# Optimization experiments

Hardware: AMD Instinct MI355X
Metric: run time of the kernel (lower is better)

Reference implementation:

```python
import jax, jax.numpy as jnp
import numpy as np

B, C_IN, H, T = 64, 256, 512, 1024
TMAX = 1024
EPS = 1e-5  # torch LayerNorm default


def setup_inputs() -> dict:
    key = jax.random.key(0)
    ks = jax.random.split(key, 8)
    std = 1.0 / np.sqrt(H)
    u = lambda k, shape: jax.random.uniform(k, shape, jnp.float32, -std, std)
    xs = jax.random.normal(ks[0], (B, C_IN, T), jnp.float32)
    # Linear weights (torch layout [out, in]); LayerNorm gamma=0.1, beta=0,
    # except h2h beta[H:2H] = log(Uniform(1, Tmax-1))  (chrono-style init).
    def ln_h2h_bias(k):
        b = jnp.zeros((3 * H,), jnp.float32)
        z = jnp.log(jax.random.uniform(k, (H,), jnp.float32, 1.0, TMAX - 1.0))
        return b.at[H:2 * H].set(z)
    gamma = jnp.full((3 * H,), 0.1, jnp.float32)
    beta0 = jnp.zeros((3 * H,), jnp.float32)
    return {
        "xs": xs,
        "Wx0": u(ks[1], (3 * H, C_IN)), "Wh0": u(ks[2], (3 * H, H)),
        "gx0": gamma, "bx0": beta0, "gh0": gamma, "bh0": ln_h2h_bias(ks[3]),
        "Wx1": u(ks[4], (3 * H, H)), "Wh1": u(ks[5], (3 * H, H)),
        "gx1": gamma, "bx1": beta0, "gh1": gamma, "bh1": ln_h2h_bias(ks[6]),
    }


def _ln(z, g, b):
    m = jnp.mean(z, axis=-1, keepdims=True)
    v = jnp.mean((z - m) ** 2, axis=-1, keepdims=True)
    return (z - m) * jax.lax.rsqrt(v + EPS) * g + b


def _cell(x, h, Wx, Wh, gx, bx, gh, bh):
    gate_x = _ln(x @ Wx.T, gx, bx)          # [B, 3H]
    gate_h = _ln(h @ Wh.T, gh, bh)          # [B, 3H]
    i_r, i_i, i_n = jnp.split(gate_x, 3, axis=-1)
    h_r, h_i, h_n = jnp.split(gate_h, 3, axis=-1)
    r = jax.nn.sigmoid(i_r + h_r)
    ig = jax.nn.sigmoid(i_i + h_i)
    n = jnp.tanh(i_n + r * h_n)
    return n + ig * (h - n)


def reference(xs, Wx0, Wh0, gx0, bx0, gh0, bh0, Wx1, Wh1, gx1, bx1, gh1, bh1):
    p0 = (Wx0, Wh0, gx0, bx0, gh0, bh0)
    p1 = (Wx1, Wh1, gx1, bx1, gh1, bh1)
    xs_t = jnp.transpose(xs, (2, 0, 1))  # [T, B, C_IN]
    h_init = (jnp.zeros((B, H), xs.dtype), jnp.zeros((B, H), xs.dtype))

    def step(carry, x):
        h0, h1 = carry
        h0 = _cell(x, h0, *p0)
        h1 = _cell(h0, h1, *p1)
        return (h0, h1), h1

    _, ys = jax.lax.scan(step, h_init, xs_t)  # [T, B, H]
    return jnp.transpose(ys, (1, 2, 0))       # [B, H, T]
```

## Files before the change

### kernel.cpp

```cpp
#include <hip/hip_runtime.h>
#include <hip/hip_bf16.h>
#include <cstdint>
#include <cstddef>


#define NBATCH 64
#define HDIM   512
#define THREE_H 1536
#define CINDIM 256
#define T_STEPS 1024
#define EPSLN 1e-5f
#define NBLK 64

typedef __bf16 bf8v __attribute__((ext_vector_type(8)));
typedef float f4 __attribute__((ext_vector_type(4)));
typedef float f2 __attribute__((ext_vector_type(2)));
typedef unsigned int u32x4 __attribute__((ext_vector_type(4)));

static constexpr size_t OFF_BAR    = 0;
static constexpr size_t OFF_ST0P   = 8192;
static constexpr size_t OFF_ST1P   = 24576;
static constexpr size_t OFF_ST2P   = 40960;
static constexpr size_t OFF_H0BF   = 57344;
static constexpr size_t OFF_H1BF   = 122880;
static constexpr size_t OFF_STATSX = 188416;
static constexpr size_t OFF_WH0HI  = 712704;
static constexpr size_t OFF_WH0LO  = OFF_WH0HI + 1572864;
static constexpr size_t OFF_WX1HI  = OFF_WH0LO + 1572864;
static constexpr size_t OFF_WX1LO  = OFF_WX1HI + 1572864;
static constexpr size_t OFF_WH1HI  = OFF_WX1LO + 1572864;
static constexpr size_t OFF_WH1LO  = OFF_WH1HI + 1572864;
static constexpr size_t OFF_WX0HI  = OFF_WH1LO + 1572864;
static constexpr size_t OFF_WX0LO  = OFF_WX0HI + 786432;
static constexpr size_t OFF_XST    = OFF_WX0LO + 786432;
static constexpr size_t OFF_GX0    = OFF_XST + 33554432;

__device__ __forceinline__ f4 mf(bf8v a, bf8v b, f4 c){
  return __builtin_amdgcn_mfma_f32_16x16x32_bf16(a, b, c, 0, 0, 0);
}
__device__ __forceinline__ float sigf(float x){ return 1.0f/(1.0f + __expf(-x)); }
__device__ __forceinline__ float tanhfast(float x){ return 1.0f - 2.0f/(__expf(2.0f*x) + 1.0f); }

__device__ __forceinline__ bf8v ld16_cross(const void* p){
  u32x4 t;
  asm volatile("global_load_dwordx4 %0, %1, off sc0 sc1" : "=v"(t) : "v"(p));
  return __builtin_bit_cast(bf8v, t);
}
__device__ __forceinline__ f4 ld16f_cross(const float* p){
  f4 v;
  asm volatile("global_load_dwordx4 %0, %1, off sc0 sc1" : "=v"(v) : "v"(p));
  return v;
}
__device__ __forceinline__ void st2_cross(__hip_bfloat16* p, unsigned int u){
  asm volatile("global_store_short %0, %1, off sc0 sc1" :: "v"(p), "v"(u));
}
__device__ __forceinline__ void st8f_cross(float* p, f2 v){
  asm volatile("global_store_dwordx2 %0, %1, off sc0 sc1" :: "v"(p), "v"(v));
}
__device__ __forceinline__ void vm_drain(){
  asm volatile("s_waitcnt vmcnt(0)" ::: "memory");
  __builtin_amdgcn_sched_barrier(0);
}

__device__ __forceinline__ void gbar(unsigned int* flags, unsigned int target){
  asm volatile("s_waitcnt vmcnt(0) lgkmcnt(0)" ::: "memory");
  __syncthreads();
  if (threadIdx.x == 0){
    unsigned int* myf = flags + (size_t)blockIdx.x * 32;
    asm volatile("global_store_dword %0, %1, off sc0 sc1" :: "v"(myf), "v"(target) : "memory");
  }
  const int lane = threadIdx.x & 63;
  const unsigned int* pf = flags + (size_t)lane * 32;
  for (;;){
    unsigned int v;
    asm volatile("global_load_dword %0, %1, off sc0 sc1\n\ts_waitcnt vmcnt(0)"
                 : "=v"(v) : "v"(pf) : "memory");
    if (__all((int)(v >= target))) break;
    __builtin_amdgcn_s_sleep(1);
  }
}

__global__ void k_zero(unsigned int* p, int nwords){
  for (int i = blockIdx.x*blockDim.x + threadIdx.x; i < nwords; i += gridDim.x*blockDim.x)
    p[i] = 0u;
}

__global__ void k_conv(const float* __restrict__ src, __hip_bfloat16* __restrict__ hi,
                       __hip_bfloat16* __restrict__ lo, int n){
  for (int i = blockIdx.x*blockDim.x + threadIdx.x; i < n; i += gridDim.x*blockDim.x){
    float w = src[i];
    __hip_bfloat16 h = __float2bfloat16(w);
    hi[i] = h;
    lo[i] = __float2bfloat16(w - __bfloat162float(h));
  }
}

__global__ void k_tr(const float* __restrict__ xs, __hip_bfloat16* __restrict__ xsT){
  const int total = NBATCH * CINDIM * (T_STEPS/4);
  for (int idx = blockIdx.x*blockDim.x + threadIdx.x; idx < total; idx += gridDim.x*blockDim.x){
    int b  = idx >> 16;
    int c  = (idx >> 8) & 255;
    int t4 = idx & 255;
    const float4 v = *(const float4*)(xs + ((size_t)b*CINDIM + c)*T_STEPS + t4*4);
    float vv[4] = {v.x, v.y, v.z, v.w};
    #pragma unroll
    for (int i = 0; i < 4; ++i)
      xsT[(size_t)(4*t4 + i)*(NBATCH*CINDIM) + b*CINDIM + c] = __float2bfloat16(vv[i]);
  }
}

__global__ __launch_bounds__(256,1) void k_xgemm(unsigned char* __restrict__ ws){
  const int tid = threadIdx.x;
  const int bx = blockIdx.x;
  const int t = bx >> 4, s = bx & 15;
  const int lane = tid & 63, w = tid >> 6, l15 = lane & 15, lg = lane >> 4;

  const __hip_bfloat16* X  = (const __hip_bfloat16*)(ws + OFF_XST) + (size_t)t*(NBATCH*CINDIM);
  const __hip_bfloat16* WH = (const __hip_bfloat16*)(ws + OFF_WX0HI);
  const __hip_bfloat16* WL = (const __hip_bfloat16*)(ws + OFF_WX0LO);
  float* statsX = (float*)(ws + OFF_STATSX);
  __hip_bfloat16* GX0 = (__hip_bfloat16*)(ws + OFF_GX0) + (size_t)t*(NBATCH*THREE_H);

  __shared__ __hip_bfloat16 SB[2][2][96][72];

  f4 acc[6];
  #pragma unroll
  for (int i = 0; i < 6; ++i) acc[i] = f4{0.f,0.f,0.f,0.f};

  bf8v A0[8];
  #pragma unroll
  for (int kk = 0; kk < 8; ++kk)
    A0[kk] = *(const bf8v*)(X + (16*w + l15)*CINDIM + kk*32 + 8*lg);

  bf8v pre[6];
  #pragma unroll
  for (int rep = 0; rep < 6; ++rep){
    int idx = tid + rep*256; int half = idx >= 768 ? 1 : 0; int i2 = idx - half*768;
    int rr = i2 >> 3, ko = (i2 & 7)*8;
    int j = 32*s + (rr & 31) + 512*(rr >> 5);
    const __hip_bfloat16* sp = (half ? WL : WH) + (size_t)j*CINDIM;
    pre[rep] = *(const bf8v*)(sp + ko);
  }
  #pragma unroll
  for (int chk = 0; chk < 4; ++chk){
    #pragma unroll
    for (int rep = 0; rep < 6; ++rep){
      int idx = tid + rep*256; int half = idx >= 768 ? 1 : 0; int i2 = idx - half*768;
      int rr = i2 >> 3, ko = (i2 & 7)*8;
      *(bf8v*)&SB[chk & 1][half][rr][ko] = pre[rep];
    }
    __syncthreads();
    if (chk < 3){
      #pragma unroll
      for (int rep = 0; rep < 6; ++rep){
        int idx = tid + rep*256; int half = idx >= 768 ? 1 : 0; int i2 = idx - half*768;
        int rr = i2 >> 3, ko = (i2 & 7)*8;
        int j = 32*s + (rr & 31) + 512*(rr >> 5);
        const __hip_bfloat16* sp = (half ? WL : WH) + (size_t)j*CINDIM;
        pre[rep] = *(const bf8v*)(sp + (chk+1)*64 + ko);
      }
    }
    #pragma unroll
    for (int sub = 0; sub < 2; ++sub){
      int kk = 2*chk + sub; int ko = 32*sub + 8*lg;
      bf8v a = A0[kk];
      #pragma unroll
      for (int nf = 0; nf < 6; ++nf){
        bf8v bh = *(const bf8v*)&SB[chk & 1][0][16*nf + l15][ko];
        bf8v bl = *(const bf8v*)&SB[chk & 1][1][16*nf + l15][ko];
        acc[nf] = mf(a, bh, acc[nf]);
        acc[nf] = mf(a, bl, acc[nf]);
      }
    }
  }

  #pragma unroll
  for (int r = 0; r < 4; ++r){
    int row = 16*w + 4*lg + r;
    float sm = 0.f, sq = 0.f;
    #pragma unroll
    for (int nf = 0; nf < 6; ++nf){
      float v = acc[nf][r];
      sm += v; sq += v*v;
      int tc = 16*nf + l15;
      int j = 32*s + (tc & 31) + 512*(tc >> 5);
      GX0[(size_t)row*THREE_H + j] = __float2bfloat16(v);
    }
    #pragma unroll
    for (int m = 1; m < 16; m <<= 1){ sm += __shfl_xor(sm, m); sq += __shfl_xor(sq, m); }
    if (l15 == 0){
      atomicAdd(&statsX[((size_t)t*64 + row)*2 + 0], sm);
      atomicAdd(&statsX[((size_t)t*64 + row)*2 + 1], sq);
    }
  }
}

__global__ void k_statsx(float* __restrict__ sx){
  int i = blockIdx.x*blockDim.x + threadIdx.x;
  if (i < T_STEPS*NBATCH){
    float s = sx[2*i], q = sx[2*i+1];
    float m = s * (1.0f/1536.0f);
    float v = fmaxf(q * (1.0f/1536.0f) - m*m, 0.0f);
    sx[2*i] = m;
    sx[2*i+1] = rsqrtf(v + EPSLN);
  }
}


__device__ __forceinline__ void runA(
    int s, unsigned char* ws, f4* red, f2* BC0,
    const float* gxg, const float* gxb, const float* ghg, const float* ghb)
{
  const int tid = threadIdx.x, lane = tid & 63, w = tid >> 6;
  const int l15 = lane & 15, lg = (lane >> 4) & 3;

  unsigned int* flags = (unsigned int*)(ws + OFF_BAR);
  float* st0P = (float*)(ws + OFF_ST0P);
  __hip_bfloat16* h0bf = (__hip_bfloat16*)(ws + OFF_H0BF);
  const float* statsX = (const float*)(ws + OFF_STATSX);
  const __hip_bfloat16* GX0 = (const __hip_bfloat16*)(ws + OFF_GX0);

  bf8v BW[3][4][2];
  {
    const __hip_bfloat16* hi = (const __hip_bfloat16*)(ws + OFF_WH0HI);
    const __hip_bfloat16* lo = (const __hip_bfloat16*)(ws + OFF_WH0LO);
    #pragma unroll
    for (int g = 0; g < 3; ++g){
      const size_t j = (size_t)(16*s + l15 + 512*g);
      #pragma unroll
      for (int kt = 0; kt < 4; ++kt){
        const size_t ko = (size_t)((4*w + kt)*32 + 8*lg);
        BW[g][kt][0] = *(const bf8v*)(hi + j*HDIM + ko);
        BW[g][kt][1] = *(const bf8v*)(lo + j*HDIM + ko);
      }
    }
  }
  float PXg[3], PXb[3], PHg[3], PHb[3];
  #pragma unroll
  for (int g = 0; g < 3; ++g){
    int j = 16*s + l15 + 512*g;
    PXg[g] = gxg[j]; PXb[g] = gxb[j]; PHg[g] = ghg[j]; PHb[g] = ghb[j];
  }

  float hp[4] = {0.f,0.f,0.f,0.f};
  unsigned int bc = 0;

  for (int tau = 0; tau <= T_STEPS; ++tau){
    const bool act = (tau < T_STEPS);
    f4 zx[3];
    float gxraw[3][4], mxv[4], rsxv[4];

    if (act){
      bf8v AR[4][4];
      #pragma unroll
      for (int rt = 0; rt < 4; ++rt)
        #pragma unroll
        for (int kt = 0; kt < 4; ++kt)
          AR[rt][kt] = ld16_cross(h0bf + (size_t)(16*rt + l15)*HDIM + (4*w + kt)*32 + 8*lg);
      vm_drain();

      f4 AC[3][4];
      #pragma unroll
      for (int g = 0; g < 3; ++g)
        #pragma unroll
        for (int rt = 0; rt < 4; ++rt) AC[g][rt] = f4{0.f,0.f,0.f,0.f};
      #pragma unroll
      for (int kt = 0; kt < 4; ++kt)
        #pragma unroll
        for (int g = 0; g < 3; ++g)
          #pragma unroll
          for (int rt = 0; rt < 4; ++rt){
            AC[g][rt] = mf(AR[rt][kt], BW[g][kt][0], AC[g][rt]);
            AC[g][rt] = mf(AR[rt][kt], BW[g][kt][1], AC[g][rt]);
          }

      #pragma unroll
      for (int r = 0; r < 4; ++r){
        int row = 16*w + 4*lg + r;
        mxv[r]  = statsX[((size_t)tau*64 + row)*2 + 0];
        rsxv[r] = statsX[((size_t)tau*64 + row)*2 + 1];
        #pragma unroll
        for (int g = 0; g < 3; ++g)
          gxraw[g][r] = __bfloat162float(
            GX0[(size_t)tau*(NBATCH*THREE_H) + (size_t)row*THREE_H + (16*s + l15 + 512*g)]);
      }

      #pragma unroll
      for (int g = 0; g < 3; ++g)
        #pragma unroll
        for (int rt = 0; rt < 4; ++rt)
          red[((w*3 + g)*4 + rt)*64 + lane] = AC[g][rt];
      __syncthreads();
      #pragma unroll
      for (int g = 0; g < 3; ++g){
        f4 a = red[((0*3 + g)*4 + w)*64 + lane];
        a += red[((1*3 + g)*4 + w)*64 + lane];
        a += red[((2*3 + g)*4 + w)*64 + lane];
        a += red[((3*3 + g)*4 + w)*64 + lane];
        zx[g] = a;
      }

      #pragma unroll
      for (int r = 0; r < 4; ++r){
        float s1 = zx[0][r] + zx[1][r] + zx[2][r];
        float q1 = zx[0][r]*zx[0][r] + zx[1][r]*zx[1][r] + zx[2][r]*zx[2][r];
        #pragma unroll
        for (int m = 1; m < 16; m <<= 1){ s1 += __shfl_xor(s1, m); q1 += __shfl_xor(q1, m); }
        if (l15 == 0){
          int row = 16*w + 4*lg + r;
          st8f_cross(st0P + ((size_t)row*32 + s)*2, f2{s1, q1});
        }
      }
    }

    gbar(flags, ++bc);

    if (act){
      {
        int row = tid >> 2, q = tid & 3;
        const float* bp = st0P + (size_t)row*64 + q*16;
        f4 v0 = ld16f_cross(bp),   v1 = ld16f_cross(bp+4);
        f4 v2 = ld16f_cross(bp+8), v3 = ld16f_cross(bp+12);
        vm_drain();
        float sm = v0[0]+v0[2]+v1[0]+v1[2]+v2[0]+v2[2]+v3[0]+v3[2];
        float sq = v0[1]+v0[3]+v1[1]+v1[3]+v2[1]+v2[3]+v3[1]+v3[3];
        sm += __shfl_xor(sm,1); sq += __shfl_xor(sq,1);
        sm += __shfl_xor(sm,2); sq += __shfl_xor(sq,2);
        if (q == 0){
          float m = sm*(1.0f/1536.0f);
          float vv = fmaxf(sq*(1.0f/1536.0f) - m*m, 0.0f);
          BC0[row] = f2{m, rsqrtf(vv + EPSLN)};
        }
      }
      __syncthreads();
      #pragma unroll
      for (int r = 0; r < 4; ++r){
        int row = 16*w + 4*lg + r;
        f2 mr = BC0[row];
        float m = mr[0], rs = mr[1];
        float ghr = (zx[0][r]-m)*rs*PHg[0] + PHb[0];
        float ghi = (zx[1][r]-m)*rs*PHg[1] + PHb[1];
        float ghn = (zx[2][r]-m)*rs*PHg[2] + PHb[2];
        float gxr = (gxraw[0][r] - mxv[r])*rsxv[r]*PXg[0] + PXb[0];
        float gxi = (gxraw[1][r] - mxv[r])*rsxv[r]*PXg[1] + PXb[1];
        float gxn = (gxraw[2][r] - mxv[r])*rsxv[r]*PXg[2] + PXb[2];
        float rg = sigf(gxr + ghr);
        float ig = sigf(gxi + ghi);
        float nn = tanhfast(gxn + rg*ghn);
        float hn = nn + ig*(hp[r] - nn);
        hp[r] = hn;
        __hip_bfloat16 hb = __float2bfloat16(hn);
        st2_cross(h0bf + (size_t)row*HDIM + 16*s + l15,
                  (unsigned int)*reinterpret_cast<unsigned short*>(&hb));
      }
    }

    gbar(flags, ++bc);
  }
}

__device__ __forceinline__ void runB(
    int s, unsigned char* ws, f4* red, f2* BC1, f2* BC2,
    const float* gxg, const float* gxb, const float* ghg, const float* ghb,
    float* out)
{
  const int tid = threadIdx.x, lane = tid & 63, w = tid >> 6;
  const int l15 = lane & 15, lg = (lane >> 4) & 3;

  unsigned int* flags = (unsigned int*)(ws + OFF_BAR);
  float* st1P = (float*)(ws + OFF_ST1P);
  float* st2P = (float*)(ws + OFF_ST2P);
  __hip_bfloat16* h0bf = (__hip_bfloat16*)(ws + OFF_H0BF);
  __hip_bfloat16* h1bf = (__hip_bfloat16*)(ws + OFF_H1BF);

  bf8v BW[6][4][2];
  {
    const __hip_bfloat16* hix = (const __hip_bfloat16*)(ws + OFF_WX1HI);
    const __hip_bfloat16* lox = (const __hip_bfloat16*)(ws + OFF_WX1LO);
    const __hip_bfloat16* hih = (const __hip_bfloat16*)(ws + OFF_WH1HI);
    const __hip_bfloat16* loh = (const __hip_bfloat16*)(ws + OFF_WH1LO);
    #pragma unroll
    for (int g = 0; g < 3; ++g){
      const size_t j = (size_t)(16*s + l15 + 512*g);
      #pragma unroll
      for (int kt = 0; kt < 4; ++kt){
        const size_t ko = (size_t)((4*w + kt)*32 + 8*lg);
        BW[g][kt][0]   = *(const bf8v*)(hix + j*HDIM + ko);
        BW[g][kt][1]   = *(const bf8v*)(lox + j*HDIM + ko);
        BW[3+g][kt][0] = *(const bf8v*)(hih + j*HDIM + ko);
        BW[3+g][kt][1] = *(const bf8v*)(loh + j*HDIM + ko);
      }
    }
  }
  float PXg[3], PXb[3], PHg[3], PHb[3];
  #pragma unroll
  for (int g = 0; g < 3; ++g){
    int j = 16*s + l15 + 512*g;
    PXg[g] = gxg[j]; PXb[g] = gxb[j]; PHg[g] = ghg[j]; PHb[g] = ghb[j];
  }

  float hp[4] = {0.f,0.f,0.f,0.f};
  unsigned int bc = 0;

  for (int tau = 0; tau <= T_STEPS; ++tau){
    const bool act = (tau >= 1);
    f4 zx[3], zh[3];

    if (act){
      bf8v AR[4][4];
      #pragma unroll
      for (int rt = 0; rt < 4; ++rt)
        #pragma unroll
        for (int kt = 0; kt < 4; ++kt)
          AR[rt][kt] = ld16_cross(h0bf + (size_t)(16*rt + l15)*HDIM + (4*w + kt)*32 + 8*lg);
      vm_drain();

      f4 AC[3][4];
      #pragma unroll
      for (int g = 0; g < 3; ++g)
        #pragma unroll
        for (int rt = 0; rt < 4; ++rt) AC[g][rt] = f4{0.f,0.f,0.f,0.f};
      #pragma unroll
      for (int kt = 0; kt < 4; ++kt)
        #pragma unroll
        for (int g = 0; g < 3; ++g)
          #pragma unroll
          for (int rt = 0; rt < 4; ++rt){
            AC[g][rt] = mf(AR[rt][kt], BW[g][kt][0], AC[g][rt]);
            AC[g][rt] = mf(AR[rt][kt], BW[g][kt][1], AC[g][rt]);
          }
      #pragma unroll
      for (int g = 0; g < 3; ++g)
        #pragma unroll
        for (int rt = 0; rt < 4; ++rt)
          red[((w*3 + g)*4 + rt)*64 + lane] = AC[g][rt];

      #pragma unroll
      for (int rt = 0; rt < 4; ++rt)
        #pragma unroll
        for (int kt = 0; kt < 4; ++kt)
          AR[rt][kt] = ld16_cross(h1bf + (size_t)(16*rt + l15)*HDIM + (4*w + kt)*32 + 8*lg);

      __syncthreads();
      #pragma unroll
      for (int g = 0; g < 3; ++g){
        f4 a = red[((0*3 + g)*4 + w)*64 + lane];
        a += red[((1*3 + g)*4 + w)*64 + lane];
        a += red[((2*3 + g)*4 + w)*64 + lane];
        a += red[((3*3 + g)*4 + w)*64 + lane];
        zx[g] = a;
      }
      __syncthreads();

      vm_drain();
      #pragma unroll
      for (int g = 0; g < 3; ++g)
        #pragma unroll
        for (int rt = 0; rt < 4; ++rt) AC[g][rt] = f4{0.f,0.f,0.f,0.f};
      #pragma unroll
      for (int kt = 0; kt < 4; ++kt)
        #pragma unroll
        for (int g = 0; g < 3; ++g)
          #pragma unroll
          for (int rt = 0; rt < 4; ++rt){
            AC[g][rt] = mf(AR[rt][kt], BW[3+g][kt][0], AC[g][rt]);
            AC[g][rt] = mf(AR[rt][kt], BW[3+g][kt][1], AC[g][rt]);
          }
      #pragma unroll
      for (int g = 0; g < 3; ++g)
        #pragma unroll
        for (int rt = 0; rt < 4; ++rt)
          red[((w*3 + g)*4 + rt)*64 + lane] = AC[g][rt];
      __syncthreads();
      #pragma unroll
      for (int g = 0; g < 3; ++g){
        f4 a = red[((0*3 + g)*4 + w)*64 + lane];
        a += red[((1*3 + g)*4 + w)*64 + lane];
        a += red[((2*3 + g)*4 + w)*64 + lane];
        a += red[((3*3 + g)*4 + w)*64 + lane];
        zh[g] = a;
      }

      #pragma unroll
      for (int r = 0; r < 4; ++r){
        float s1 = zx[0][r] + zx[1][r] + zx[2][r];
        float q1 = zx[0][r]*zx[0][r] + zx[1][r]*zx[1][r] + zx[2][r]*zx[2][r];
        float s2 = zh[0][r] + zh[1][r] + zh[2][r];
        float q2 = zh[0][r]*zh[0][r] + zh[1][r]*zh[1][r] + zh[2][r]*zh[2][r];
        #pragma unroll
        for (int m = 1; m < 16; m <<= 1){
          s1 += __shfl_xor(s1, m); q1 += __shfl_xor(q1, m);
          s2 += __shfl_xor(s2, m); q2 += __shfl_xor(q2, m);
        }
        if (l15 == 0){
          int row = 16*w + 4*lg + r;
          st8f_cross(st1P + ((size_t)row*32 + s)*2, f2{s1, q1});
          st8f_cross(st2P + ((size_t)row*32 + s)*2, f2{s2, q2});
        }
      }
    }

    gbar(flags, ++bc);

    if (act){
      const int t1 = tau - 1;
      {
        int row = tid >> 2, q = tid & 3;
        const float* b1 = st1P + (size_t)row*64 + q*16;
        const float* b2 = st2P + (size_t)row*64 + q*16;
        f4 a0 = ld16f_cross(b1),   a1 = ld16f_cross(b1+4);
        f4 a2 = ld16f_cross(b1+8), a3 = ld16f_cross(b1+12);
        f4 c0 = ld16f_cross(b2),   c1 = ld16f_cross(b2+4);
        f4 c2 = ld16f_cross(b2+8), c3 = ld16f_cross(b2+12);
        vm_drain();
        float s1 = a0[0]+a0[2]+a1[0]+a1[2]+a2[0]+a2[2]+a3[0]+a3[2];
        float q1 = a0[1]+a0[3]+a1[1]+a1[3]+a2[1]+a2[3]+a3[1]+a3[3];
        float s2 = c0[0]+c0[2]+c1[0]+c1[2]+c2[0]+c2[2]+c3[0]+c3[2];
        float q2 = c0[1]+c0[3]+c1[1]+c1[3]+c2[1]+c2[3]+c3[1]+c3[3];
        s1 += __shfl_xor(s1,1); q1 += __shfl_xor(q1,1);
        s1 += __shfl_xor(s1,2); q1 += __shfl_xor(q1,2);
        s2 += __shfl_xor(s2,1); q2 += __shfl_xor(q2,1);
        s2 += __shfl_xor(s2,2); q2 += __shfl_xor(q2,2);
        if (q == 0){
          float m1 = s1*(1.0f/1536.0f);
          float v1 = fmaxf(q1*(1.0f/1536.0f) - m1*m1, 0.0f);
          BC1[row] = f2{m1, rsqrtf(v1 + EPSLN)};
          float m2 = s2*(1.0f/1536.0f);
          float v2 = fmaxf(q2*(1.0f/1536.0f) - m2*m2, 0.0f);
          BC2[row] = f2{m2, rsqrtf(v2 + EPSLN)};
        }
      }
      __syncthreads();
      #pragma unroll
      for (int r = 0; r < 4; ++r){
        int row = 16*w + 4*lg + r;
        f2 m1 = BC1[row], m2 = BC2[row];
        float gxr = (zx[0][r] - m1[0])*m1[1]*PXg[0] + PXb[0];
        float gxi = (zx[1][r] - m1[0])*m1[1]*PXg[1] + PXb[1];
        float gxn = (zx[2][r] - m1[0])*m1[1]*PXg[2] + PXb[2];
        float ghr = (zh[0][r] - m2[0])*m2[1]*PHg[0] + PHb[0];
        float ghi = (zh[1][r] - m2[0])*m2[1]*PHg[1] + PHb[1];
        float ghn = (zh[2][r] - m2[0])*m2[1]*PHg[2] + PHb[2];
        float rg = sigf(gxr + ghr);
        float ig = sigf(gxi + ghi);
        float nn = tanhfast(gxn + rg*ghn);
        float hn = nn + ig*(hp[r] - nn);
        hp[r] = hn;
        int j = 16*s + l15;
        __hip_bfloat16 hb = __float2bfloat16(hn);
        st2_cross(h1bf + (size_t)row*HDIM + j,
                  (unsigned int)*reinterpret_cast<unsigned short*>(&hb));
        out[(size_t)row*(HDIM*T_STEPS) + (size_t)j*T_STEPS + t1] = hn;
      }
    }

    gbar(flags, ++bc);
  }
}

__global__ __launch_bounds__(256,1) void k_rnn(
    const float* __restrict__ gx0g, const float* __restrict__ gx0b,
    const float* __restrict__ gh0g, const float* __restrict__ gh0b,
    const float* __restrict__ gx1g, const float* __restrict__ gx1b,
    const float* __restrict__ gh1g, const float* __restrict__ gh1b,
    unsigned char* __restrict__ ws, float* __restrict__ out)
{
  __shared__ f4 red[4*3*4*64];
  __shared__ f2 BCa[64];
  __shared__ f2 BCb[64];

  const int bi = blockIdx.x;
  if (bi < 32)
    runA(bi, ws, red, BCa, gx0g, gx0b, gh0g, gh0b);
  else
    runB(bi - 32, ws, red, BCa, BCb, gx1g, gx1b, gh1g, gh1b, out);
}

extern "C" void kernel_launch(void* const* d_in, const int* in_sizes, int n_in,
                              void* d_out, int out_size, void* d_ws, size_t ws_size,
                              hipStream_t stream) {
  const float* xs  = (const float*)d_in[0];
  const float* Wx0 = (const float*)d_in[1];
  const float* Wh0 = (const float*)d_in[2];
  const float* gx0g = (const float*)d_in[3];
  const float* gx0b = (const float*)d_in[4];
  const float* gh0g = (const float*)d_in[5];
  const float* gh0b = (const float*)d_in[6];
  const float* Wx1 = (const float*)d_in[7];
  const float* Wh1 = (const float*)d_in[8];
  const float* gx1g = (const float*)d_in[9];
  const float* gx1b = (const float*)d_in[10];
  const float* gh1g = (const float*)d_in[11];
  const float* gh1b = (const float*)d_in[12];

  unsigned char* ws = (unsigned char*)d_ws;
  float* out = (float*)d_out;
  (void)in_sizes; (void)n_in; (void)out_size; (void)ws_size;

  k_zero<<<256, 256, 0, stream>>>((unsigned int*)ws, (int)(OFF_WH0HI/4));

  k_conv<<<512, 256, 0, stream>>>(Wh0, (__hip_bfloat16*)(ws+OFF_WH0HI), (__hip_bfloat16*)(ws+OFF_WH0LO), THREE_H*HDIM);
  k_conv<<<512, 256, 0, stream>>>(Wx1, (__hip_bfloat16*)(ws+OFF_WX1HI), (__hip_bfloat16*)(ws+OFF_WX1LO), THREE_H*HDIM);
  k_conv<<<512, 256, 0, stream>>>(Wh1, (__hip_bfloat16*)(ws+OFF_WH1HI), (__hip_bfloat16*)(ws+OFF_WH1LO), THREE_H*HDIM);
  k_conv<<<512, 256, 0, stream>>>(Wx0, (__hip_bfloat16*)(ws+OFF_WX0HI), (__hip_bfloat16*)(ws+OFF_WX0LO), THREE_H*CINDIM);

  k_tr<<<4096, 256, 0, stream>>>(xs, (__hip_bfloat16*)(ws+OFF_XST));

  k_xgemm<<<16384, 256, 0, stream>>>(ws);
  k_statsx<<<256, 256, 0, stream>>>((float*)(ws+OFF_STATSX));

  k_rnn<<<NBLK, 256, 0, stream>>>(gx0g, gx0b, gh0g, gh0b, gx1g, gx1b, gh1g, gh1b, ws, out);
}
```

Before: 13.02 ms.

## Replace per-step stats barriers with epoch-tagged partial polling and double-buffered hidden states

Partial LayerNorm sums are now written as 16-byte records tagged with the step index. Consumers spin on those tags instead of passing through a grid-wide flag barrier, which removes one of the two global barriers per time step. The hidden-state buffers for both layers are double-buffered by step parity so the remaining barrier still orders reads against writes. Layer B's final step is peeled out of the loop. The cost is more workspace, polling traffic on the stats arrays, and reliance on the float tag and the write landing atomically.

```diff
diff --git a/kernel.cpp b/kernel.cpp
--- a/kernel.cpp
+++ b/kernel.cpp
@@ -11,6 +11,7 @@
 #define T_STEPS 1024
 #define EPSLN 1e-5f
 #define NBLK 64
+#define HSZ (NBATCH*HDIM)
 
 typedef __bf16 bf8v __attribute__((ext_vector_type(8)));
 typedef float f4 __attribute__((ext_vector_type(4)));
@@ -18,13 +19,13 @@
 typedef unsigned int u32x4 __attribute__((ext_vector_type(4)));
 
 static constexpr size_t OFF_BAR    = 0;
-static constexpr size_t OFF_ST0P   = 8192;
-static constexpr size_t OFF_ST1P   = 24576;
-static constexpr size_t OFF_ST2P   = 40960;
-static constexpr size_t OFF_H0BF   = 57344;
-static constexpr size_t OFF_H1BF   = 122880;
-static constexpr size_t OFF_STATSX = 188416;
-static constexpr size_t OFF_WH0HI  = 712704;
+static constexpr size_t OFF_STA    = 8192;
+static constexpr size_t OFF_STB1   = 40960;
+static constexpr size_t OFF_STB2   = 73728;
+static constexpr size_t OFF_H0BF   = 106496;
+static constexpr size_t OFF_H1BF   = 237568;
+static constexpr size_t OFF_STATSX = 368640;
+static constexpr size_t OFF_WH0HI  = 892928;
 static constexpr size_t OFF_WH0LO  = OFF_WH0HI + 1572864;
 static constexpr size_t OFF_WX1HI  = OFF_WH0LO + 1572864;
 static constexpr size_t OFF_WX1LO  = OFF_WX1HI + 1572864;
@@ -51,11 +52,17 @@
   asm volatile("global_load_dwordx4 %0, %1, off sc0 sc1" : "=v"(v) : "v"(p));
   return v;
 }
+__device__ __forceinline__ f4 ld16f_poll(const float* p){
+  f4 v;
+  asm volatile("global_load_dwordx4 %0, %1, off sc0 sc1\n\ts_waitcnt vmcnt(0)"
+               : "=v"(v) : "v"(p) : "memory");
+  return v;
+}
 __device__ __forceinline__ void st2_cross(__hip_bfloat16* p, unsigned int u){
   asm volatile("global_store_short %0, %1, off sc0 sc1" :: "v"(p), "v"(u));
 }
-__device__ __forceinline__ void st8f_cross(float* p, f2 v){
-  asm volatile("global_store_dwordx2 %0, %1, off sc0 sc1" :: "v"(p), "v"(v));
+__device__ __forceinline__ void st16f_cross(float* p, f4 v){
+  asm volatile("global_store_dwordx4 %0, %1, off sc0 sc1" :: "v"(p), "v"(v));
 }
 __device__ __forceinline__ void vm_drain(){
   asm volatile("s_waitcnt vmcnt(0)" ::: "memory");
@@ -215,7 +222,7 @@
   const int l15 = lane & 15, lg = (lane >> 4) & 3;
 
   unsigned int* flags = (unsigned int*)(ws + OFF_BAR);
-  float* st0P = (float*)(ws + OFF_ST0P);
+  float* stA = (float*)(ws + OFF_STA);
   __hip_bfloat16* h0bf = (__hip_bfloat16*)(ws + OFF_H0BF);
   const float* statsX = (const float*)(ws + OFF_STATSX);
   const __hip_bfloat16* GX0 = (const __hip_bfloat16*)(ws + OFF_GX0);
@@ -245,114 +252,121 @@
   float hp[4] = {0.f,0.f,0.f,0.f};
   unsigned int bc = 0;
 
-  for (int tau = 0; tau <= T_STEPS; ++tau){
-    const bool act = (tau < T_STEPS);
+  for (int tau = 0; tau < T_STEPS; ++tau){
+    const float ef = (float)(tau + 1);
+    const __hip_bfloat16* h0r = h0bf + (size_t)((tau + 1) & 1) * HSZ;
+    __hip_bfloat16*       h0w = h0bf + (size_t)(tau & 1) * HSZ;
+
     f4 zx[3];
     float gxraw[3][4], mxv[4], rsxv[4];
 
-    if (act){
-      bf8v AR[4][4];
+    bf8v AR[4][4];
+    #pragma unroll
+    for (int rt = 0; rt < 4; ++rt)
+      #pragma unroll
+      for (int kt = 0; kt < 4; ++kt)
+        AR[rt][kt] = ld16_cross(h0r + (size_t)(16*rt + l15)*HDIM + (4*w + kt)*32 + 8*lg);
+    vm_drain();
+
+    f4 AC[3][4];
+    #pragma unroll
+    for (int g = 0; g < 3; ++g)
+      #pragma unroll
+      for (int rt = 0; rt < 4; ++rt) AC[g][rt] = f4{0.f,0.f,0.f,0.f};
+    #pragma unroll
+    for (int kt = 0; kt < 4; ++kt)
+      #pragma unroll
+      for (int g = 0; g < 3; ++g)
+        #pragma unroll
+        for (int rt = 0; rt < 4; ++rt){
+          AC[g][rt] = mf(AR[rt][kt], BW[g][kt][0], AC[g][rt]);
+          AC[g][rt] = mf(AR[rt][kt], BW[g][kt][1], AC[g][rt]);
+        }
+
+    #pragma unroll
+    for (int r = 0; r < 4; ++r){
+      int row = 16*w + 4*lg + r;
+      mxv[r]  = statsX[((size_t)tau*64 + row)*2 + 0];
+      rsxv[r] = statsX[((size_t)tau*64 + row)*2 + 1];
+      #pragma unroll
+      for (int g = 0; g < 3; ++g)
+        gxraw[g][r] = __bfloat162float(
+          GX0[(size_t)tau*(NBATCH*THREE_H) + (size_t)row*THREE_H + (16*s + l15 + 512*g)]);
+    }
+
+    #pragma unroll
+    for (int g = 0; g < 3; ++g)
       #pragma unroll
       for (int rt = 0; rt < 4; ++rt)
-        #pragma unroll
-        for (int kt = 0; kt < 4; ++kt)
-          AR[rt][kt] = ld16_cross(h0bf + (size_t)(16*rt + l15)*HDIM + (4*w + kt)*32 + 8*lg);
-      vm_drain();
-
-      f4 AC[3][4];
-      #pragma unroll
-      for (int g = 0; g < 3; ++g)
-        #pragma unroll
-        for (int rt = 0; rt < 4; ++rt) AC[g][rt] = f4{0.f,0.f,0.f,0.f};
-      #pragma unroll
-      for (int kt = 0; kt < 4; ++kt)
-        #pragma unroll
-        for (int g = 0; g < 3; ++g)
-          #pragma unroll
-          for (int rt = 0; rt < 4; ++rt){
-            AC[g][rt] = mf(AR[rt][kt], BW[g][kt][0], AC[g][rt]);
-            AC[g][rt] = mf(AR[rt][kt], BW[g][kt][1], AC[g][rt]);
-          }
-
-      #pragma unroll
-      for (int r = 0; r < 4; ++r){
+        red[((w*3 + g)*4 + rt)*64 + lane] = AC[g][rt];
+    __syncthreads();
+    #pragma unroll
+    for (int g = 0; g < 3; ++g){
+      f4 a = red[((0*3 + g)*4 + w)*64 + lane];
+      a += red[((1*3 + g)*4 + w)*64 + lane];
+      a += red[((2*3 + g)*4 + w)*64 + lane];
+      a += red[((3*3 + g)*4 + w)*64 + lane];
+      zx[g] = a;
+    }
+
+    #pragma unroll
+    for (int r = 0; r < 4; ++r){
+      float s1 = zx[0][r] + zx[1][r] + zx[2][r];
+      float q1 = zx[0][r]*zx[0][r] + zx[1][r]*zx[1][r] + zx[2][r]*zx[2][r];
+      #pragma unroll
+      for (int m = 1; m < 16; m <<= 1){ s1 += __shfl_xor(s1, m); q1 += __shfl_xor(q1, m); }
+      if (l15 == 0){
         int row = 16*w + 4*lg + r;
-        mxv[r]  = statsX[((size_t)tau*64 + row)*2 + 0];
-        rsxv[r] = statsX[((size_t)tau*64 + row)*2 + 1];
-        #pragma unroll
-        for (int g = 0; g < 3; ++g)
-          gxraw[g][r] = __bfloat162float(
-            GX0[(size_t)tau*(NBATCH*THREE_H) + (size_t)row*THREE_H + (16*s + l15 + 512*g)]);
-      }
-
-      #pragma unroll
-      for (int g = 0; g < 3; ++g)
-        #pragma unroll
-        for (int rt = 0; rt < 4; ++rt)
-          red[((w*3 + g)*4 + rt)*64 + lane] = AC[g][rt];
-      __syncthreads();
-      #pragma unroll
-      for (int g = 0; g < 3; ++g){
-        f4 a = red[((0*3 + g)*4 + w)*64 + lane];
-        a += red[((1*3 + g)*4 + w)*64 + lane];
-        a += red[((2*3 + g)*4 + w)*64 + lane];
-        a += red[((3*3 + g)*4 + w)*64 + lane];
-        zx[g] = a;
-      }
-
-      #pragma unroll
-      for (int r = 0; r < 4; ++r){
-        float s1 = zx[0][r] + zx[1][r] + zx[2][r];
-        float q1 = zx[0][r]*zx[0][r] + zx[1][r]*zx[1][r] + zx[2][r]*zx[2][r];
-        #pragma unroll
-        for (int m = 1; m < 16; m <<= 1){ s1 += __shfl_xor(s1, m); q1 += __shfl_xor(q1, m); }
-        if (l15 == 0){
-          int row = 16*w + 4*lg + r;
-          st8f_cross(st0P + ((size_t)row*32 + s)*2, f2{s1, q1});
-        }
-      }
-    }
-
-    gbar(flags, ++bc);
-
-    if (act){
-      {
-        int row = tid >> 2, q = tid & 3;
-        const float* bp = st0P + (size_t)row*64 + q*16;
-        f4 v0 = ld16f_cross(bp),   v1 = ld16f_cross(bp+4);
-        f4 v2 = ld16f_cross(bp+8), v3 = ld16f_cross(bp+12);
-        vm_drain();
-        float sm = v0[0]+v0[2]+v1[0]+v1[2]+v2[0]+v2[2]+v3[0]+v3[2];
-        float sq = v0[1]+v0[3]+v1[1]+v1[3]+v2[1]+v2[3]+v3[1]+v3[3];
-        sm += __shfl_xor(sm,1); sq += __shfl_xor(sq,1);
-        sm += __shfl_xor(sm,2); sq += __shfl_xor(sq,2);
-        if (q == 0){
-          float m = sm*(1.0f/1536.0f);
-          float vv = fmaxf(sq*(1.0f/1536.0f) - m*m, 0.0f);
-          BC0[row] = f2{m, rsqrtf(vv + EPSLN)};
-        }
-      }
-      __syncthreads();
-      #pragma unroll
-      for (int r = 0; r < 4; ++r){
-        int row = 16*w + 4*lg + r;
-        f2 mr = BC0[row];
-        float m = mr[0], rs = mr[1];
-        float ghr = (zx[0][r]-m)*rs*PHg[0] + PHb[0];
-        float ghi = (zx[1][r]-m)*rs*PHg[1] + PHb[1];
-        float ghn = (zx[2][r]-m)*rs*PHg[2] + PHb[2];
-        float gxr = (gxraw[0][r] - mxv[r])*rsxv[r]*PXg[0] + PXb[0];
-        float gxi = (gxraw[1][r] - mxv[r])*rsxv[r]*PXg[1] + PXb[1];
-        float gxn = (gxraw[2][r] - mxv[r])*rsxv[r]*PXg[2] + PXb[2];
-        float rg = sigf(gxr + ghr);
-        float ig = sigf(gxi + ghi);
-        float nn = tanhfast(gxn + rg*ghn);
-        float hn = nn + ig*(hp[r] - nn);
-        hp[r] = hn;
-        __hip_bfloat16 hb = __float2bfloat16(hn);
-        st2_cross(h0bf + (size_t)row*HDIM + 16*s + l15,
-                  (unsigned int)*reinterpret_cast<unsigned short*>(&hb));
-      }
+        st16f_cross(stA + ((size_t)row*32 + s)*4, f4{s1, q1, ef, 0.f});
+      }
+    }
+
+    {
+      int row = tid >> 2, q = tid & 3;
+      const float* bp = stA + ((size_t)row*32 + q*8)*4;
+      f4 v[8];
+      for (;;){
+        bool ok = true;
+        #pragma unroll
+        for (int i = 0; i < 8; ++i){
+          v[i] = ld16f_poll(bp + i*4);
+          ok = ok && (v[i][2] == ef);
+        }
+        if (__all((int)ok)) break;
+        __builtin_amdgcn_s_sleep(1);
+      }
+      float sm = 0.f, sq = 0.f;
+      #pragma unroll
+      for (int i = 0; i < 8; ++i){ sm += v[i][0]; sq += v[i][1]; }
+      sm += __shfl_xor(sm,1); sq += __shfl_xor(sq,1);
+      sm += __shfl_xor(sm,2); sq += __shfl_xor(sq,2);
+      if (q == 0){
+        float m = sm*(1.0f/1536.0f);
+        float vv = fmaxf(sq*(1.0f/1536.0f) - m*m, 0.0f);
+        BC0[row] = f2{m, rsqrtf(vv + EPSLN)};
+      }
+    }
+    __syncthreads();
+
+    #pragma unroll
+    for (int r = 0; r < 4; ++r){
+      int row = 16*w + 4*lg + r;
+      f2 mr = BC0[row];
+      float m = mr[0], rs = mr[1];
+      float ghr = (zx[0][r]-m)*rs*PHg[0] + PHb[0];
+      float ghi = (zx[1][r]-m)*rs*PHg[1] + PHb[1];
+      float ghn = (zx[2][r]-m)*rs*PHg[2] + PHb[2];
+      float gxr = (gxraw[0][r] - mxv[r])*rsxv[r]*PXg[0] + PXb[0];
+      float gxi = (gxraw[1][r] - mxv[r])*rsxv[r]*PXg[1] + PXb[1];
+      float gxn = (gxraw[2][r] - mxv[r])*rsxv[r]*PXg[2] + PXb[2];
+      float rg = sigf(gxr + ghr);
+      float ig = sigf(gxi + ghi);
+      float nn = tanhfast(gxn + rg*ghn);
+      float hn = nn + ig*(hp[r] - nn);
+      hp[r] = hn;
+      __hip_bfloat16 hb = __float2bfloat16(hn);
+      st2_cross(h0w + (size_t)row*HDIM + 16*s + l15,
+                (unsigned int)*reinterpret_cast<unsigned short*>(&hb));
     }
 
     gbar(flags, ++bc);
@@ -368,8 +382,8 @@
   const int l15 = lane & 15, lg = (lane >> 4) & 3;
 
   unsigned int* flags = (unsigned int*)(ws + OFF_BAR);
-  float* st1P = (float*)(ws + OFF_ST1P);
-  float* st2P = (float*)(ws + OFF_ST2P);
+  float* stB1 = (float*)(ws + OFF_STB1);
+  float* stB2 = (float*)(ws + OFF_STB2);
   __hip_bfloat16* h0bf = (__hip_bfloat16*)(ws + OFF_H0BF);
   __hip_bfloat16* h1bf = (__hip_bfloat16*)(ws + OFF_H1BF);
 
@@ -402,8 +416,13 @@
   float hp[4] = {0.f,0.f,0.f,0.f};
   unsigned int bc = 0;
 
-  for (int tau = 0; tau <= T_STEPS; ++tau){
+  for (int tau = 0; tau < T_STEPS; ++tau){
     const bool act = (tau >= 1);
+    const float ef = (float)tau;
+    const __hip_bfloat16* h0r = h0bf + (size_t)((tau + 1) & 1) * HSZ;
+    const __hip_bfloat16* h1r = h1bf + (size_t)((tau + 1) & 1) * HSZ;
+    __hip_bfloat16*       h1w = h1bf + (size_t)(tau & 1) * HSZ;
+
     f4 zx[3], zh[3];
 
     if (act){
@@ -412,7 +431,7 @@
       for (int rt = 0; rt < 4; ++rt)
         #pragma unroll
         for (int kt = 0; kt < 4; ++kt)
-          AR[rt][kt] = ld16_cross(h0bf + (size_t)(16*rt + l15)*HDIM + (4*w + kt)*32 + 8*lg);
+          AR[rt][kt] = ld16_cross(h0r + (size_t)(16*rt + l15)*HDIM + (4*w + kt)*32 + 8*lg);
       vm_drain();
 
       f4 AC[3][4];
@@ -439,7 +458,7 @@
       for (int rt = 0; rt < 4; ++rt)
         #pragma unroll
         for (int kt = 0; kt < 4; ++kt)
-          AR[rt][kt] = ld16_cross(h1bf + (size_t)(16*rt + l15)*HDIM + (4*w + kt)*32 + 8*lg);
+          AR[rt][kt] = ld16_cross(h1r + (size_t)(16*rt + l15)*HDIM + (4*w + kt)*32 + 8*lg);
 
       __syncthreads();
       #pragma unroll
@@ -494,43 +513,49 @@
         }
         if (l15 == 0){
           int row = 16*w + 4*lg + r;
-          st8f_cross(st1P + ((size_t)row*32 + s)*2, f2{s1, q1});
-          st8f_cross(st2P + ((size_t)row*32 + s)*2, f2{s2, q2});
-        }
-      }
-    }
-
-    gbar(flags, ++bc);
-
-    if (act){
-      const int t1 = tau - 1;
+          st16f_cross(stB1 + ((size_t)row*32 + s)*4, f4{s1, q1, ef, 0.f});
+          st16f_cross(stB2 + ((size_t)row*32 + s)*4, f4{s2, q2, ef, 0.f});
+        }
+      }
+
       {
         int row = tid >> 2, q = tid & 3;
-        const float* b1 = st1P + (size_t)row*64 + q*16;
-        const float* b2 = st2P + (size_t)row*64 + q*16;
-        f4 a0 = ld16f_cross(b1),   a1 = ld16f_cross(b1+4);
-        f4 a2 = ld16f_cross(b1+8), a3 = ld16f_cross(b1+12);
-        f4 c0 = ld16f_cross(b2),   c1 = ld16f_cross(b2+4);
-        f4 c2 = ld16f_cross(b2+8), c3 = ld16f_cross(b2+12);
-        vm_drain();
-        float s1 = a0[0]+a0[2]+a1[0]+a1[2]+a2[0]+a2[2]+a3[0]+a3[2];
-        float q1 = a0[1]+a0[3]+a1[1]+a1[3]+a2[1]+a2[3]+a3[1]+a3[3];
-        float s2 = c0[0]+c0[2]+c1[0]+c1[2]+c2[0]+c2[2]+c3[0]+c3[2];
-        float q2 = c0[1]+c0[3]+c1[1]+c1[3]+c2[1]+c2[3]+c3[1]+c3[3];
+        const float* b1 = stB1 + ((size_t)row*32 + q*8)*4;
+        const float* b2 = stB2 + ((size_t)row*32 + q*8)*4;
+        f4 v1[8], v2[8];
+        for (;;){
+          bool ok = true;
+          #pragma unroll
+          for (int i = 0; i < 8; ++i){
+            v1[i] = ld16f_poll(b1 + i*4);
+            v2[i] = ld16f_poll(b2 + i*4);
+            ok = ok && (v1[i][2] == ef) && (v2[i][2] == ef);
+          }
+          if (__all((int)ok)) break;
+          __builtin_amdgcn_s_sleep(1);
+        }
+        float s1 = 0.f, q1 = 0.f, s2 = 0.f, q2 = 0.f;
+        #pragma unroll
+        for (int i = 0; i < 8; ++i){
+          s1 += v1[i][0]; q1 += v1[i][1];
+          s2 += v2[i][0]; q2 += v2[i][1];
+        }
         s1 += __shfl_xor(s1,1); q1 += __shfl_xor(q1,1);
         s1 += __shfl_xor(s1,2); q1 += __shfl_xor(q1,2);
         s2 += __shfl_xor(s2,1); q2 += __shfl_xor(q2,1);
         s2 += __shfl_xor(s2,2); q2 += __shfl_xor(q2,2);
         if (q == 0){
           float m1 = s1*(1.0f/1536.0f);
-          float v1 = fmaxf(q1*(1.0f/1536.0f) - m1*m1, 0.0f);
-          BC1[row] = f2{m1, rsqrtf(v1 + EPSLN)};
+          float vv1 = fmaxf(q1*(1.0f/1536.0f) - m1*m1, 0.0f);
+          BC1[row] = f2{m1, rsqrtf(vv1 + EPSLN)};
           float m2 = s2*(1.0f/1536.0f);
-          float v2 = fmaxf(q2*(1.0f/1536.0f) - m2*m2, 0.0f);
-          BC2[row] = f2{m2, rsqrtf(v2 + EPSLN)};
+          float vv2 = fmaxf(q2*(1.0f/1536.0f) - m2*m2, 0.0f);
+          BC2[row] = f2{m2, rsqrtf(vv2 + EPSLN)};
         }
       }
       __syncthreads();
+
+      const int t1 = tau - 1;
       #pragma unroll
       for (int r = 0; r < 4; ++r){
         int row = 16*w + 4*lg + r;
@@ -548,13 +573,162 @@
         hp[r] = hn;
         int j = 16*s + l15;
         __hip_bfloat16 hb = __float2bfloat16(hn);
-        st2_cross(h1bf + (size_t)row*HDIM + j,
+        st2_cross(h1w + (size_t)row*HDIM + j,
                   (unsigned int)*reinterpret_cast<unsigned short*>(&hb));
         out[(size_t)row*(HDIM*T_STEPS) + (size_t)j*T_STEPS + t1] = hn;
       }
     }
 
     gbar(flags, ++bc);
+  }
+
+  {
+    const int tau = T_STEPS;
+    const float ef = (float)tau;
+    const __hip_bfloat16* h0r = h0bf + (size_t)((tau + 1) & 1) * HSZ;
+    const __hip_bfloat16* h1r = h1bf + (size_t)((tau + 1) & 1) * HSZ;
+
+    f4 zx[3], zh[3];
+    bf8v AR[4][4];
+    #pragma unroll
+    for (int rt = 0; rt < 4; ++rt)
+      #pragma unroll
+      for (int kt = 0; kt < 4; ++kt)
+        AR[rt][kt] = ld16_cross(h0r + (size_t)(16*rt + l15)*HDIM + (4*w + kt)*32 + 8*lg);
+    vm_drain();
+    f4 AC[3][4];
+    #pragma unroll
+    for (int g = 0; g < 3; ++g)
+      #pragma unroll
+      for (int rt = 0; rt < 4; ++rt) AC[g][rt] = f4{0.f,0.f,0.f,0.f};
+    #pragma unroll
+    for (int kt = 0; kt < 4; ++kt)
+      #pragma unroll
+      for (int g = 0; g < 3; ++g)
+        #pragma unroll
+        for (int rt = 0; rt < 4; ++rt){
+          AC[g][rt] = mf(AR[rt][kt], BW[g][kt][0], AC[g][rt]);
+          AC[g][rt] = mf(AR[rt][kt], BW[g][kt][1], AC[g][rt]);
+        }
+    #pragma unroll
+    for (int g = 0; g < 3; ++g)
+      #pragma unroll
+      for (int rt = 0; rt < 4; ++rt)
+        red[((w*3 + g)*4 + rt)*64 + lane] = AC[g][rt];
+    #pragma unroll
+    for (int rt = 0; rt < 4; ++rt)
+      #pragma unroll
+      for (int kt = 0; kt < 4; ++kt)
+        AR[rt][kt] = ld16_cross(h1r + (size_t)(16*rt + l15)*HDIM + (4*w + kt)*32 + 8*lg);
+    __syncthreads();
+    #pragma unroll
+    for (int g = 0; g < 3; ++g){
+      f4 a = red[((0*3 + g)*4 + w)*64 + lane];
+      a += red[((1*3 + g)*4 + w)*64 + lane];
+      a += red[((2*3 + g)*4 + w)*64 + lane];
+      a += red[((3*3 + g)*4 + w)*64 + lane];
+      zx[g] = a;
+    }
+    __syncthreads();
+    vm_drain();
+    #pragma unroll
+    for (int g = 0; g < 3; ++g)
+      #pragma unroll
+      for (int rt = 0; rt < 4; ++rt) AC[g][rt] = f4{0.f,0.f,0.f,0.f};
+    #pragma unroll
+    for (int kt = 0; kt < 4; ++kt)
+      #pragma unroll
+      for (int g = 0; g < 3; ++g)
+        #pragma unroll
+        for (int rt = 0; rt < 4; ++rt){
+          AC[g][rt] = mf(AR[rt][kt], BW[3+g][kt][0], AC[g][rt]);
+          AC[g][rt] = mf(AR[rt][kt], BW[3+g][kt][1], AC[g][rt]);
+        }
+    #pragma unroll
+    for (int g = 0; g < 3; ++g)
+      #pragma unroll
+      for (int rt = 0; rt < 4; ++rt)
+        red[((w*3 + g)*4 + rt)*64 + lane] = AC[g][rt];
+    __syncthreads();
+    #pragma unroll
+    for (int g = 0; g < 3; ++g){
+      f4 a = red[((0*3 + g)*4 + w)*64 + lane];
+      a += red[((1*3 + g)*4 + w)*64 + lane];
+      a += red[((2*3 + g)*4 + w)*64 + lane];
+      a += red[((3*3 + g)*4 + w)*64 + lane];
+      zh[g] = a;
+    }
+    #pragma unroll
+    for (int r = 0; r < 4; ++r){
+      float s1 = zx[0][r] + zx[1][r] + zx[2][r];
+      float q1 = zx[0][r]*zx[0][r] + zx[1][r]*zx[1][r] + zx[2][r]*zx[2][r];
+      float s2 = zh[0][r] + zh[1][r] + zh[2][r];
+      float q2 = zh[0][r]*zh[0][r] + zh[1][r]*zh[1][r] + zh[2][r]*zh[2][r];
+      #pragma unroll
+      for (int m = 1; m < 16; m <<= 1){
+        s1 += __shfl_xor(s1, m); q1 += __shfl_xor(q1, m);
+        s2 += __shfl_xor(s2, m); q2 += __shfl_xor(q2, m);
+      }
+      if (l15 == 0){
+        int row = 16*w + 4*lg + r;
+        st16f_cross(stB1 + ((size_t)row*32 + s)*4, f4{s1, q1, ef, 0.f});
+        st16f_cross(stB2 + ((size_t)row*32 + s)*4, f4{s2, q2, ef, 0.f});
+      }
+    }
+    {
+      int row = tid >> 2, q = tid & 3;
+      const float* b1 = stB1 + ((size_t)row*32 + q*8)*4;
+      const float* b2 = stB2 + ((size_t)row*32 + q*8)*4;
+      f4 v1[8], v2[8];
+      for (;;){
+        bool ok = true;
+        #pragma unroll
+        for (int i = 0; i < 8; ++i){
+          v1[i] = ld16f_poll(b1 + i*4);
+          v2[i] = ld16f_poll(b2 + i*4);
+          ok = ok && (v1[i][2] == ef) && (v2[i][2] == ef);
+        }
+        if (__all((int)ok)) break;
+        __builtin_amdgcn_s_sleep(1);
+      }
+      float s1 = 0.f, q1 = 0.f, s2 = 0.f, q2 = 0.f;
+      #pragma unroll
+      for (int i = 0; i < 8; ++i){
+        s1 += v1[i][0]; q1 += v1[i][1];
+        s2 += v2[i][0]; q2 += v2[i][1];
+      }
+      s1 += __shfl_xor(s1,1); q1 += __shfl_xor(q1,1);
+      s1 += __shfl_xor(s1,2); q1 += __shfl_xor(q1,2);
+      s2 += __shfl_xor(s2,1); q2 += __shfl_xor(q2,1);
+      s2 += __shfl_xor(s2,2); q2 += __shfl_xor(q2,2);
+      if (q == 0){
+        float m1 = s1*(1.0f/1536.0f);
+        float vv1 = fmaxf(q1*(1.0f/1536.0f) - m1*m1, 0.0f);
+        BC1[row] = f2{m1, rsqrtf(vv1 + EPSLN)};
+        float m2 = s2*(1.0f/1536.0f);
+        float vv2 = fmaxf(q2*(1.0f/1536.0f) - m2*m2, 0.0f);
+        BC2[row] = f2{m2, rsqrtf(vv2 + EPSLN)};
+      }
+    }
+    __syncthreads();
+    const int t1 = T_STEPS - 1;
+    #pragma unroll
+    for (int r = 0; r < 4; ++r){
+      int row = 16*w + 4*lg + r;
+      f2 m1 = BC1[row], m2 = BC2[row];
+      float gxr = (zx[0][r] - m1[0])*m1[1]*PXg[0] + PXb[0];
+      float gxi = (zx[1][r] - m1[0])*m1[1]*PXg[1] + PXb[1];
+      float gxn = (zx[2][r] - m1[0])*m1[1]*PXg[2] + PXb[2];
+      float ghr = (zh[0][r] - m2[0])*m2[1]*PHg[0] + PHb[0];
+      float ghi = (zh[1][r] - m2[0])*m2[1]*PHg[1] + PHb[1];
+      float ghn = (zh[2][r] - m2[0])*m2[1]*PHg[2] + PHb[2];
+      float rg = sigf(gxr + ghr);
+      float ig = sigf(gxi + ghi);
+      float nn = tanhfast(gxn + rg*ghn);
+      float hn = nn + ig*(hp[r] - nn);
+      int j = 16*s + l15;
+      out[(size_t)row*(HDIM*T_STEPS) + (size_t)j*T_STEPS + t1] = hn;
+    }
   }
 }
 
```

After: 16.77 ms. 1.29x slower.
